# Kernel optimization log

Hardware: AMD Instinct MI355X
Metric: run time of the kernel (lower is better)

The kernel has to match this reference:

```python
import jax, jax.numpy as jnp
import numpy as np

N_REF = 4

def setup_inputs() -> dict:
    key = jax.random.key(0)
    ks = jax.random.split(key, 6)
    B, C, H, W = 4, 256, 64, 64
    s = 1.0 / np.sqrt(C)
    return {
        'x': jax.random.normal(ks[0], (B, C, H, W), jnp.float32),
        'Wq': jax.random.normal(ks[1], (C, C), jnp.float32) * s,
        'bq': jnp.zeros((C,), jnp.float32),
        'Wk': jax.random.normal(ks[2], (C, C), jnp.float32) * s,
        'bk': jnp.zeros((C,), jnp.float32),
        'Wv': jax.random.normal(ks[3], (C, C), jnp.float32) * s,
        'bv': jnp.zeros((C,), jnp.float32),
        'Woff': jax.random.normal(ks[4], (2 * N_REF, C), jnp.float32) * s,
        'boff': jnp.zeros((2 * N_REF,), jnp.float32),
    }

def _proj(x, W, b):
    # 1x1 conv == channel-mixing linear: [B,C,H,W] -> [B,O,H,W]
    return jnp.einsum('oc,bchw->bohw', W, x) + b[None, :, None, None]

def reference(x, Wq, bq, Wk, bk, Wv, bv, Woff, boff):
    B, C, H, W = x.shape
    n = N_REF
    HW = H * W
    Q = _proj(x, Wq, bq)
    K = _proj(x, Wk, bk)
    V = _proj(x, Wv, bv)
    offsets = _proj(Q, Woff, boff).reshape(B, n, 2, H, W)
    grid_h, grid_w = jnp.meshgrid(jnp.arange(H), jnp.arange(W), indexing='ij')
    ref_x = jnp.clip(jnp.round(grid_w[None, None] + offsets[:, :, 0]).astype(jnp.int32), 0, W - 1)
    ref_y = jnp.clip(jnp.round(grid_h[None, None] + offsets[:, :, 1]).astype(jnp.int32), 0, H - 1)
    ref_idx = (ref_y * W + ref_x).reshape(B, n, HW)          # [B,n,HW]
    K_flat = K.reshape(B, C, HW)
    V_flat = V.reshape(B, C, HW)
    # gather along spatial dim -> [B,C,n,HW]
    idx = ref_idx[:, None, :, :]                              # [B,1,n,HW]
    K_g = jnp.take_along_axis(K_flat[:, :, None, :], idx, axis=3)
    V_g = jnp.take_along_axis(V_flat[:, :, None, :], idx, axis=3)
    Q_flat = Q.reshape(B, C, HW)
    attn = jnp.einsum('bch,bcnh->bnh', Q_flat, K_g)
    attn = jax.nn.softmax(attn, axis=1)
    out = jnp.einsum('bnh,bcnh->bch', attn, V_g)
    return out.reshape(B, C, H, W)
```

## Files before the change

kernel.cpp:

```cpp
#include <hip/hip_runtime.h>
#include <math.h>

#define B_DIM   4
#define C_DIM   256
#define H_DIM   64
#define W_DIM   64
#define HW_DIM  4096
#define NPIX    (B_DIM * HW_DIM)
#define NREF    4
#define NJ      10

typedef unsigned short u16;
typedef __attribute__((ext_vector_type(4))) unsigned short u16x4;
typedef __attribute__((ext_vector_type(8))) unsigned short u16x8;
typedef __attribute__((ext_vector_type(8))) short bf16x8;
typedef __attribute__((ext_vector_type(4))) float f32x4;

__device__ __forceinline__ u16 bf16_rne(float f) {
    unsigned u = __float_as_uint(f);
    u = u + 0x7FFFu + ((u >> 16) & 1u);
    return (u16)(u >> 16);
}
__device__ __forceinline__ float bf16_tof(u16 h) {
    return __uint_as_float(((unsigned)h) << 16);
}
__device__ __forceinline__ void gload16(const void* g, void* l) {
    __builtin_amdgcn_global_load_lds(
        (const __attribute__((address_space(1))) void*)g,
        (__attribute__((address_space(3))) void*)l, 16, 0, 0);
}

__global__ __launch_bounds__(256) void prep_kernel(
    const float* __restrict__ Wq, const float* __restrict__ bq,
    const float* __restrict__ Wk, const float* __restrict__ bk,
    const float* __restrict__ Wv,
    const float* __restrict__ Woff, const float* __restrict__ boff,
    double* __restrict__ Weffp, double* __restrict__ beff,
    u16* __restrict__ Bswh, u16* __restrict__ Bswl)
{
    const int bx = blockIdx.x;
    const int t  = threadIdx.x;

    if (bx < 4 * NJ) {
        const int j  = bx >> 2;
        const int q  = bx & 3;
        const int o0 = q * 64;
        const float* Avec = (j < 8) ? (Woff + j * C_DIM) : ((j == 8) ? bq : bk);
        const float* Bmat = (j == 8) ? Wk : Wq;
        double s0 = 0, s1 = 0, s2 = 0, s3 = 0;
        for (int o = o0; o < o0 + 64; o += 4) {
            s0 += (double)Avec[o + 0] * (double)Bmat[(size_t)(o + 0) * C_DIM + t];
            s1 += (double)Avec[o + 1] * (double)Bmat[(size_t)(o + 1) * C_DIM + t];
            s2 += (double)Avec[o + 2] * (double)Bmat[(size_t)(o + 2) * C_DIM + t];
            s3 += (double)Avec[o + 3] * (double)Bmat[(size_t)(o + 3) * C_DIM + t];
        }
        Weffp[(size_t)(q * NJ + j) * C_DIM + t] = (s0 + s1) + (s2 + s3);

        if (q == 0 && j <= 8) {
            __shared__ double red[256];
            red[t] = (j < 8) ? (double)Woff[j * C_DIM + t] * (double)bq[t]
                             : (double)bq[t] * (double)bk[t];
            __syncthreads();
            for (int st = 128; st > 0; st >>= 1) {
                if (t < st) red[t] += red[t + st];
                __syncthreads();
            }
            if (t == 0) beff[j] = (j < 8) ? red[0] + (double)boff[j] : red[0];
        }
    } else if (bx < 72) {
        __shared__ float wq_s[64][32];
        __shared__ float wk_s[64][64];
        const int sub   = bx - 40;
        const int T     = sub >> 2;
        const int nsub  = sub & 3;
        const int ntile = T >> 2;
        const int kt    = T & 3;
        const int nb    = ntile * 128 + nsub * 32;
        const int kb    = kt * 64;

        const int tx = t & 15;
        const int ty = t >> 4;

        float acc[2][4] = {};

        for (int oc = 0; oc < 4; ++oc) {
            const int o0 = oc * 64;
#pragma unroll
            for (int i = 0; i < 2; ++i) {
                const int s = i * 256 + t;
                const int row = s >> 3, c4 = (s & 7) * 4;
                *(float4*)&wq_s[row][c4] =
                    *(const float4*)(Wq + (size_t)(o0 + row) * C_DIM + nb + c4);
            }
#pragma unroll
            for (int i = 0; i < 4; ++i) {
                const int s = i * 256 + t;
                const int row = s >> 4, c4 = (s & 15) * 4;
                *(float4*)&wk_s[row][c4] =
                    *(const float4*)(Wk + (size_t)(o0 + row) * C_DIM + kb + c4);
            }
            __syncthreads();
#pragma unroll 4
            for (int oo = 0; oo < 64; ++oo) {
                const float2 a = *(const float2*)&wq_s[oo][ty * 2];
                const float4 b4 = *(const float4*)&wk_s[oo][tx * 4];
                acc[0][0] = fmaf(a.x, b4.x, acc[0][0]);
                acc[0][1] = fmaf(a.x, b4.y, acc[0][1]);
                acc[0][2] = fmaf(a.x, b4.z, acc[0][2]);
                acc[0][3] = fmaf(a.x, b4.w, acc[0][3]);
                acc[1][0] = fmaf(a.y, b4.x, acc[1][0]);
                acc[1][1] = fmaf(a.y, b4.y, acc[1][1]);
                acc[1][2] = fmaf(a.y, b4.z, acc[1][2]);
                acc[1][3] = fmaf(a.y, b4.w, acc[1][3]);
            }
            __syncthreads();
        }

        u16* dh = Bswh + (size_t)T * 8192;
        u16* dl = Bswl + (size_t)T * 8192;
#pragma unroll
        for (int j = 0; j < 2; ++j) {
            const int rimg = nsub * 32 + ty * 2 + j;
            const int base = rimg * 64 + (((tx >> 1) ^ (rimg & 7)) * 8) + (tx & 1) * 4;
            u16x4 hv, lv;
#pragma unroll
            for (int i = 0; i < 4; ++i) {
                hv[i] = bf16_rne(acc[j][i]);
                lv[i] = bf16_rne(acc[j][i] - bf16_tof(hv[i]));
            }
            *(u16x4*)(dh + base) = hv;
            *(u16x4*)(dl + base) = lv;
        }
    } else {
        const int ti    = bx - 72;
        const int kt    = ti & 3;
        const int ntile = (ti >> 2) & 1;
        const int Timg  = 8 + ti;
        const int n0 = ntile * 128, k0 = kt * 64;
        u16* dh = Bswh + (size_t)Timg * 8192;
#pragma unroll
        for (int it = 0; it < 4; ++it) {
            const int s   = it * 256 + t;
            const int row = s >> 3;
            const int ch  = s & 7;
            const int kk  = k0 + (ch ^ (row & 7)) * 8;
            const float4 w0 = *(const float4*)(Wv + (size_t)(n0 + row) * C_DIM + kk);
            const float4 w1 = *(const float4*)(Wv + (size_t)(n0 + row) * C_DIM + kk + 4);
            u16x8 hv;
            hv[0] = bf16_rne(w0.x); hv[1] = bf16_rne(w0.y);
            hv[2] = bf16_rne(w0.z); hv[3] = bf16_rne(w0.w);
            hv[4] = bf16_rne(w1.x); hv[5] = bf16_rne(w1.y);
            hv[6] = bf16_rne(w1.z); hv[7] = bf16_rne(w1.w);
            *(u16x8*)(dh + (size_t)s * 8) = hv;
        }
    }
}

__global__ __launch_bounds__(256) void xsplit_kernel(
    const float* __restrict__ x, const double* __restrict__ Weffp,
    u16* __restrict__ xh, u16* __restrict__ xl, double* __restrict__ part)
{
    __shared__ float  tile[64][65];
    __shared__ double wf[NJ][64];
    const int b   = blockIdx.z;
    const int cy  = blockIdx.y;
    const int c0  = cy * 64;
    const int hw0 = blockIdx.x * 64;
    const int t   = threadIdx.x;
    const int r4  = t >> 6;
    const int col = t & 63;

#pragma unroll
    for (int i = 0; i < 16; ++i) {
        const int row = i * 4 + r4;
        tile[row][col] = x[((size_t)b * C_DIM + c0 + row) * HW_DIM + hw0 + col];
    }
    for (int d = t; d < NJ * 64; d += 256) {
        const int jj = d >> 6, cc = d & 63;
        ((double*)wf)[d] = Weffp[(size_t)(0 * NJ + jj) * C_DIM + c0 + cc]
                         + Weffp[(size_t)(1 * NJ + jj) * C_DIM + c0 + cc]
                         + Weffp[(size_t)(2 * NJ + jj) * C_DIM + c0 + cc]
                         + Weffp[(size_t)(3 * NJ + jj) * C_DIM + c0 + cc];
    }
    __syncthreads();

#pragma unroll
    for (int i = 0; i < 16; ++i) {
        const int hwr = i * 4 + r4;
        const float v = tile[col][hwr];
        const u16 h = bf16_rne(v);
        const float lo = v - bf16_tof(h);
        const size_t o = ((size_t)b * HW_DIM + hw0 + hwr) * C_DIM + c0 + col;
        xh[o] = h;
        xl[o] = bf16_rne(lo);
    }

    const int p = col, g = r4;
    double a0 = 0, a1 = 0, a2 = 0;
    for (int c = 0; c < 64; ++c) {
        const double xv = (double)tile[c][p];
        a0 += wf[2 * g][c] * xv;
        a1 += wf[2 * g + 1][c] * xv;
        if (g < 2) a2 += wf[8 + g][c] * xv;
    }
    const int pix = b * HW_DIM + hw0 + p;
    part[(size_t)(cy * NJ + 2 * g) * NPIX + pix]     = a0;
    part[(size_t)(cy * NJ + 2 * g + 1) * NPIX + pix] = a1;
    if (g < 2) part[(size_t)(cy * NJ + 8 + g) * NPIX + pix] = a2;
}

__global__ __launch_bounds__(256) void idx_kernel(
    const double* __restrict__ part, const double* __restrict__ beff,
    int* __restrict__ idx_buf, float* __restrict__ kqf, float* __restrict__ vqf)
{
    const int pix = blockIdx.x * 256 + threadIdx.x;
    const int hw  = pix & (HW_DIM - 1);
    const int h   = hw >> 6;
    const int w   = hw & 63;

    double o[8];
#pragma unroll
    for (int j = 0; j < 8; ++j)
        o[j] = part[(size_t)(0 * NJ + j) * NPIX + pix] + part[(size_t)(1 * NJ + j) * NPIX + pix]
             + part[(size_t)(2 * NJ + j) * NPIX + pix] + part[(size_t)(3 * NJ + j) * NPIX + pix]
             + beff[j];

    int r[NREF];
#pragma unroll
    for (int n = 0; n < NREF; ++n) {
        const float ox = (float)o[2 * n];
        const float oy = (float)o[2 * n + 1];
        int rx = (int)rintf((float)w + ox);
        int ry = (int)rintf((float)h + oy);
        rx = min(max(rx, 0), W_DIM - 1);
        ry = min(max(ry, 0), H_DIM - 1);
        r[n] = ry * W_DIM + rx;
    }
    int4 outv; outv.x = r[0]; outv.y = r[1]; outv.z = r[2]; outv.w = r[3];
    *(int4*)(idx_buf + (size_t)pix * 4) = outv;

    const double kq = part[(size_t)(0 * NJ + 8) * NPIX + pix] + part[(size_t)(1 * NJ + 8) * NPIX + pix]
                    + part[(size_t)(2 * NJ + 8) * NPIX + pix] + part[(size_t)(3 * NJ + 8) * NPIX + pix];
    const double vq = part[(size_t)(0 * NJ + 9) * NPIX + pix] + part[(size_t)(1 * NJ + 9) * NPIX + pix]
                    + part[(size_t)(2 * NJ + 9) * NPIX + pix] + part[(size_t)(3 * NJ + 9) * NPIX + pix]
                    + beff[8];
    kqf[pix] = (float)kq;
    vqf[pix] = (float)vq;
}

__global__ __launch_bounds__(256) void qkv_mfma(
    const u16* __restrict__ xh, const u16* __restrict__ xl,
    const u16* __restrict__ Bswh, const u16* __restrict__ Bswl,
    const float* __restrict__ bv,
    float* __restrict__ Kpt, u16* __restrict__ Vtb)
{
    const int mat = blockIdx.x & 1;
    const int m0  = (blockIdx.x >> 1) * 64;
    const bool three = (mat == 0);

    __shared__ u16 lds[40960];
    u16* Ah = lds;
    u16* Al = lds + 4096;
    u16* Bh = lds + 8192;
    u16* Bl = lds + 24576;

    const int t    = threadIdx.x;
    const int lane = t & 63;
    const int wv   = t >> 6;
    const int wm   = (wv >> 1) * 32;
    const int wn   = (wv & 1) * 128;

    f32x4 acc[2][8] = {};

    for (int kt = 0; kt < 4; ++kt) {
        const int k0 = kt * 64;

#pragma unroll
        for (int it = 0; it < 2; ++it) {
            const int s   = it * 256 + t;
            const int row = s >> 3;
            const int sch = (s & 7) ^ (row & 7);
            const size_t goff = (size_t)(m0 + row) * C_DIM + k0 + sch * 8;
            gload16(xh + goff, (char*)Ah + s * 16);
            if (three) gload16(xl + goff, (char*)Al + s * 16);
        }
#pragma unroll
        for (int it = 0; it < 8; ++it) {
            const int s  = it * 256 + t;
            const int ni = s >> 10;
            const int sl = s & 1023;
            const size_t Tb = (size_t)((mat * 2 + ni) * 4 + kt) * 8192;
            gload16(Bswh + Tb + (size_t)sl * 8, (char*)Bh + s * 16);
            if (three) gload16(Bswl + Tb + (size_t)sl * 8, (char*)Bl + s * 16);
        }
        __syncthreads();

#pragma unroll
        for (int ks = 0; ks < 2; ++ks) {
            bf16x8 afh[2], afl[2];
#pragma unroll
            for (int mt = 0; mt < 2; ++mt) {
                const int row = wm + mt * 16 + (lane & 15);
                const int ch  = (ks * 4 + (lane >> 4)) ^ (row & 7);
                const int off = row * 128 + ch * 16;
                afh[mt] = *(const bf16x8*)((const char*)Ah + off);
                if (three) afl[mt] = *(const bf16x8*)((const char*)Al + off);
            }
#pragma unroll
            for (int ng = 0; ng < 2; ++ng) {
                bf16x8 bfh[4], bfl[4];
#pragma unroll
                for (int nt = 0; nt < 4; ++nt) {
                    const int row = wn + ng * 64 + nt * 16 + (lane & 15);
                    const int ch  = (ks * 4 + (lane >> 4)) ^ (row & 7);
                    const int off = row * 128 + ch * 16;
                    bfh[nt] = *(const bf16x8*)((const char*)Bh + off);
                    if (three) bfl[nt] = *(const bf16x8*)((const char*)Bl + off);
                }
#pragma unroll
                for (int mt = 0; mt < 2; ++mt)
#pragma unroll
                    for (int nt = 0; nt < 4; ++nt) {
                        f32x4 a = acc[mt][ng * 4 + nt];
                        a = __builtin_amdgcn_mfma_f32_16x16x32_bf16(afh[mt], bfh[nt], a, 0, 0, 0);
                        if (three) {
                            a = __builtin_amdgcn_mfma_f32_16x16x32_bf16(afh[mt], bfl[nt], a, 0, 0, 0);
                            a = __builtin_amdgcn_mfma_f32_16x16x32_bf16(afl[mt], bfh[nt], a, 0, 0, 0);
                        }
                        acc[mt][ng * 4 + nt] = a;
                    }
            }
        }
        __syncthreads();
    }

    const int col = lane & 15;
    const int rg  = (lane >> 4) * 4;
#pragma unroll
    for (int ng = 0; ng < 2; ++ng)
#pragma unroll
        for (int nt = 0; nt < 4; ++nt) {
            const int n = wn + ng * 64 + nt * 16 + col;
            const float bias = mat ? bv[n] : 0.0f;
#pragma unroll
            for (int mt = 0; mt < 2; ++mt) {
                const int m = m0 + wm + mt * 16 + rg;
#pragma unroll
                for (int r = 0; r < 4; ++r) {
                    const float v = acc[mt][ng * 4 + nt][r] + bias;
                    if (mat) Vtb[(size_t)(m + r) * C_DIM + n] = bf16_rne(v);
                    else     Kpt[(size_t)(m + r) * C_DIM + n] = v;
                }
            }
        }
}

__global__ __launch_bounds__(1024) void attn_kernel(
    const u16*   __restrict__ xh,
    const u16*   __restrict__ xl,
    const float* __restrict__ Kpt,
    const u16*   __restrict__ Vtb,
    const int*   __restrict__ idx_buf,
    const float* __restrict__ kqf,
    const float* __restrict__ vqf,
    float* __restrict__ out)
{
    __shared__ float trans[16][260];

    const int t    = threadIdx.x;
    const int wave = t >> 6;
    const int lane = t & 63;

    const int pix0 = blockIdx.x * 16;
    const int b    = pix0 / HW_DIM;
    const int hw   = (pix0 % HW_DIM) + wave;
    const int pix  = b * HW_DIM + hw;

    const u16x4 hv = *(const u16x4*)(xh + (size_t)pix * C_DIM + lane * 4);
    const u16x4 lv = *(const u16x4*)(xl + (size_t)pix * C_DIM + lane * 4);
    float q[4];
#pragma unroll
    for (int i = 0; i < 4; ++i) q[i] = bf16_tof(hv[i]) + bf16_tof(lv[i]);

    const int4 iv = *(const int4*)(idx_buf + (size_t)pix * 4);
    int idx[NREF] = {iv.x, iv.y, iv.z, iv.w};
    const float vq = vqf[pix];

    float logit[NREF];
#pragma unroll
    for (int n = 0; n < NREF; ++n) {
        const float* krow = Kpt + ((size_t)b * HW_DIM + idx[n]) * C_DIM;
        float4 kv = *(const float4*)(krow + lane * 4);
        float lp = fmaf(q[3], kv.w, fmaf(q[2], kv.z, fmaf(q[1], kv.y, q[0] * kv.x)));
#pragma unroll
        for (int off = 1; off < 64; off <<= 1) lp += __shfl_xor(lp, off);
        logit[n] = lp + kqf[(size_t)b * HW_DIM + idx[n]] + vq;
    }

    float mx = fmaxf(fmaxf(logit[0], logit[1]), fmaxf(logit[2], logit[3]));
    float e[NREF], s = 0.0f;
#pragma unroll
    for (int n = 0; n < NREF; ++n) { e[n] = expf(logit[n] - mx); s += e[n]; }
    float wgt[NREF];
#pragma unroll
    for (int n = 0; n < NREF; ++n) wgt[n] = e[n] / s;

    float o4[4] = {0.f, 0.f, 0.f, 0.f};
#pragma unroll
    for (int n = 0; n < NREF; ++n) {
        const u16x4 vv = *(const u16x4*)(Vtb + ((size_t)b * HW_DIM + idx[n]) * C_DIM + lane * 4);
        o4[0] = fmaf(wgt[n], bf16_tof(vv[0]), o4[0]);
        o4[1] = fmaf(wgt[n], bf16_tof(vv[1]), o4[1]);
        o4[2] = fmaf(wgt[n], bf16_tof(vv[2]), o4[2]);
        o4[3] = fmaf(wgt[n], bf16_tof(vv[3]), o4[3]);
    }

    *(float4*)&trans[wave][lane * 4] = *(float4*)o4;
    __syncthreads();

    float* ob = out + (size_t)b * C_DIM * HW_DIM + (pix0 % HW_DIM);
    const int px = t & 15;
#pragma unroll
    for (int cc = 0; cc < C_DIM; cc += 64) {
        const int c = cc + (t >> 4);
        ob[(size_t)c * HW_DIM + px] = trans[px][c];
    }
}

extern "C" void kernel_launch(void* const* d_in, const int* in_sizes, int n_in,
                              void* d_out, int out_size, void* d_ws, size_t ws_size,
                              hipStream_t stream) {
    const float* x    = (const float*)d_in[0];
    const float* Wq   = (const float*)d_in[1];
    const float* bq   = (const float*)d_in[2];
    const float* Wk   = (const float*)d_in[3];
    const float* bk   = (const float*)d_in[4];
    const float* Wv   = (const float*)d_in[5];
    const float* bv   = (const float*)d_in[6];
    const float* Woff = (const float*)d_in[7];
    const float* boff = (const float*)d_in[8];
    float* out = (float*)d_out;

    char* ws = (char*)d_ws;
    float*  Kpt   = (float*)ws;
    u16*    Vtb   = (u16*)  (ws + (size_t)16 * 1024 * 1024);
    u16*    xh    = (u16*)  (ws + (size_t)48 * 1024 * 1024);
    u16*    xl    = (u16*)  (ws + (size_t)56 * 1024 * 1024);
    char*   aux   = ws + (size_t)64 * 1024 * 1024;
    double* Weffp = (double*)(aux);
    double* beff  = (double*)(aux + 128 * 1024);
    int*    idxb  = (int*)   (aux + 192 * 1024);
    float*  kqf   = (float*) (aux + 448 * 1024);
    float*  vqf   = (float*) (aux + 512 * 1024);
    u16*    Bswh  = (u16*)   (aux + 576 * 1024);
    u16*    Bswl  = (u16*)   (aux + 832 * 1024);
    double* part  = (double*)(aux + 2 * 1024 * 1024);

    prep_kernel<<<dim3(80), dim3(256), 0, stream>>>(
        Wq, bq, Wk, bk, Wv, Woff, boff, Weffp, beff, Bswh, Bswl);
    xsplit_kernel<<<dim3(HW_DIM / 64, C_DIM / 64, B_DIM), dim3(256), 0, stream>>>(
        x, Weffp, xh, xl, part);
    idx_kernel<<<dim3(NPIX / 256), dim3(256), 0, stream>>>(part, beff, idxb, kqf, vqf);
    qkv_mfma<<<dim3((NPIX / 64) * 2), dim3(256), 0, stream>>>(
        xh, xl, Bswh, Bswl, bv, Kpt, Vtb);
    attn_kernel<<<dim3(NPIX / 16), dim3(1024), 0, stream>>>(
        xh, xl, Kpt, Vtb, idxb, kqf, vqf, out);
}
```

Before: 64.67 us.

## Fuse xsplit with index computation and compute K and V in one GEMM block

The xsplit and idx kernels are merged. Each block now loops over all four channel chunks for 32 pixels and reduces the offset partial sums in shared memory, so the double-precision partial buffer round trip through global memory and one launch go away. The QKV GEMM kernel now computes both the K (three-pass split bf16) and V (single-pass) outputs for a 32-row tile inside the same block, reusing the loaded A tile. The cost is fewer pixels per block in the fused kernel, serial channel chunks with extra barriers, and a smaller M tile that lowers B-operand reuse in the GEMM.

New measurement: 105.0 us. 62.3% more time.

```diff
diff --git a/kernel.cpp b/kernel.cpp
--- a/kernel.cpp
+++ b/kernel.cpp
@@ -156,96 +156,93 @@
     }
 }
 
-__global__ __launch_bounds__(256) void xsplit_kernel(
+__global__ __launch_bounds__(256) void xsplit_idx_kernel(
     const float* __restrict__ x, const double* __restrict__ Weffp,
-    u16* __restrict__ xh, u16* __restrict__ xl, double* __restrict__ part)
-{
-    __shared__ float  tile[64][65];
-    __shared__ double wf[NJ][64];
-    const int b   = blockIdx.z;
-    const int cy  = blockIdx.y;
-    const int c0  = cy * 64;
-    const int hw0 = blockIdx.x * 64;
-    const int t   = threadIdx.x;
-    const int r4  = t >> 6;
-    const int col = t & 63;
-
-#pragma unroll
-    for (int i = 0; i < 16; ++i) {
-        const int row = i * 4 + r4;
-        tile[row][col] = x[((size_t)b * C_DIM + c0 + row) * HW_DIM + hw0 + col];
-    }
-    for (int d = t; d < NJ * 64; d += 256) {
-        const int jj = d >> 6, cc = d & 63;
-        ((double*)wf)[d] = Weffp[(size_t)(0 * NJ + jj) * C_DIM + c0 + cc]
-                         + Weffp[(size_t)(1 * NJ + jj) * C_DIM + c0 + cc]
-                         + Weffp[(size_t)(2 * NJ + jj) * C_DIM + c0 + cc]
-                         + Weffp[(size_t)(3 * NJ + jj) * C_DIM + c0 + cc];
-    }
-    __syncthreads();
-
-#pragma unroll
-    for (int i = 0; i < 16; ++i) {
-        const int hwr = i * 4 + r4;
-        const float v = tile[col][hwr];
-        const u16 h = bf16_rne(v);
-        const float lo = v - bf16_tof(h);
-        const size_t o = ((size_t)b * HW_DIM + hw0 + hwr) * C_DIM + c0 + col;
-        xh[o] = h;
-        xl[o] = bf16_rne(lo);
-    }
-
-    const int p = col, g = r4;
-    double a0 = 0, a1 = 0, a2 = 0;
-    for (int c = 0; c < 64; ++c) {
-        const double xv = (double)tile[c][p];
-        a0 += wf[2 * g][c] * xv;
-        a1 += wf[2 * g + 1][c] * xv;
-        if (g < 2) a2 += wf[8 + g][c] * xv;
-    }
-    const int pix = b * HW_DIM + hw0 + p;
-    part[(size_t)(cy * NJ + 2 * g) * NPIX + pix]     = a0;
-    part[(size_t)(cy * NJ + 2 * g + 1) * NPIX + pix] = a1;
-    if (g < 2) part[(size_t)(cy * NJ + 8 + g) * NPIX + pix] = a2;
-}
-
-__global__ __launch_bounds__(256) void idx_kernel(
-    const double* __restrict__ part, const double* __restrict__ beff,
+    const double* __restrict__ beff,
+    u16* __restrict__ xh, u16* __restrict__ xl,
     int* __restrict__ idx_buf, float* __restrict__ kqf, float* __restrict__ vqf)
 {
-    const int pix = blockIdx.x * 256 + threadIdx.x;
-    const int hw  = pix & (HW_DIM - 1);
-    const int h   = hw >> 6;
-    const int w   = hw & 63;
-
-    double o[8];
-#pragma unroll
-    for (int j = 0; j < 8; ++j)
-        o[j] = part[(size_t)(0 * NJ + j) * NPIX + pix] + part[(size_t)(1 * NJ + j) * NPIX + pix]
-             + part[(size_t)(2 * NJ + j) * NPIX + pix] + part[(size_t)(3 * NJ + j) * NPIX + pix]
-             + beff[j];
-
-    int r[NREF];
-#pragma unroll
-    for (int n = 0; n < NREF; ++n) {
-        const float ox = (float)o[2 * n];
-        const float oy = (float)o[2 * n + 1];
-        int rx = (int)rintf((float)w + ox);
-        int ry = (int)rintf((float)h + oy);
-        rx = min(max(rx, 0), W_DIM - 1);
-        ry = min(max(ry, 0), H_DIM - 1);
-        r[n] = ry * W_DIM + rx;
-    }
-    int4 outv; outv.x = r[0]; outv.y = r[1]; outv.z = r[2]; outv.w = r[3];
-    *(int4*)(idx_buf + (size_t)pix * 4) = outv;
-
-    const double kq = part[(size_t)(0 * NJ + 8) * NPIX + pix] + part[(size_t)(1 * NJ + 8) * NPIX + pix]
-                    + part[(size_t)(2 * NJ + 8) * NPIX + pix] + part[(size_t)(3 * NJ + 8) * NPIX + pix];
-    const double vq = part[(size_t)(0 * NJ + 9) * NPIX + pix] + part[(size_t)(1 * NJ + 9) * NPIX + pix]
-                    + part[(size_t)(2 * NJ + 9) * NPIX + pix] + part[(size_t)(3 * NJ + 9) * NPIX + pix]
-                    + beff[8];
-    kqf[pix] = (float)kq;
-    vqf[pix] = (float)vq;
+    __shared__ float  tile[64][33];
+    __shared__ double wf[NJ][64];
+    __shared__ double osum[NJ][32];
+
+    const int b   = blockIdx.y;
+    const int hw0 = blockIdx.x * 32;
+    const int t   = threadIdx.x;
+
+    const int p  = t & 31;
+    const int g  = t >> 5;
+    const int cl = t & 63;
+    const int gg = t >> 6;
+
+    double pj[4], pj2[4];
+
+    for (int cy = 0; cy < 4; ++cy) {
+        const int c0 = cy * 64;
+        if (cy) __syncthreads();
+
+#pragma unroll
+        for (int i = 0; i < 8; ++i) {
+            const int s = i * 256 + t;
+            const int row = s >> 5;
+            const int pp  = s & 31;
+            tile[row][pp] = x[((size_t)b * C_DIM + c0 + row) * HW_DIM + hw0 + pp];
+        }
+        for (int d = t; d < NJ * 64; d += 256) {
+            const int jj = d >> 6, cc = d & 63;
+            ((double*)wf)[d] = Weffp[(size_t)(0 * NJ + jj) * C_DIM + c0 + cc]
+                             + Weffp[(size_t)(1 * NJ + jj) * C_DIM + c0 + cc]
+                             + Weffp[(size_t)(2 * NJ + jj) * C_DIM + c0 + cc]
+                             + Weffp[(size_t)(3 * NJ + jj) * C_DIM + c0 + cc];
+        }
+        __syncthreads();
+
+#pragma unroll
+        for (int i = 0; i < 8; ++i) {
+            const int hwr = i * 4 + gg;
+            const float v = tile[cl][hwr];
+            const u16 hbits = bf16_rne(v);
+            const float lo = v - bf16_tof(hbits);
+            const size_t o = ((size_t)b * HW_DIM + hw0 + hwr) * C_DIM + c0 + cl;
+            xh[o] = hbits;
+            xl[o] = bf16_rne(lo);
+        }
+
+        double a0 = 0, a1 = 0;
+        for (int c = 0; c < 64; ++c) {
+            const double xv = (double)tile[c][p];
+            a0 += wf[g][c] * xv;
+            if (g < 2) a1 += wf[8 + g][c] * xv;
+        }
+        pj[cy]  = a0;
+        pj2[cy] = a1;
+    }
+
+    osum[g][p] = ((pj[0] + pj[1]) + pj[2]) + pj[3];
+    if (g < 2) osum[8 + g][p] = ((pj2[0] + pj2[1]) + pj2[2]) + pj2[3];
+    __syncthreads();
+
+    if (t < 32) {
+        const int hw  = hw0 + t;
+        const int pix = b * HW_DIM + hw;
+        const int h   = hw >> 6;
+        const int w   = hw & 63;
+        int r[NREF];
+#pragma unroll
+        for (int n = 0; n < NREF; ++n) {
+            const float ox = (float)(osum[2 * n][t]     + beff[2 * n]);
+            const float oy = (float)(osum[2 * n + 1][t] + beff[2 * n + 1]);
+            int rx = (int)rintf((float)w + ox);
+            int ry = (int)rintf((float)h + oy);
+            rx = min(max(rx, 0), W_DIM - 1);
+            ry = min(max(ry, 0), H_DIM - 1);
+            r[n] = ry * W_DIM + rx;
+        }
+        int4 outv; outv.x = r[0]; outv.y = r[1]; outv.z = r[2]; outv.w = r[3];
+        *(int4*)(idx_buf + (size_t)pix * 4) = outv;
+        kqf[pix] = (float)osum[8][t];
+        vqf[pix] = (float)(osum[9][t] + beff[8]);
+    }
 }
 
 __global__ __launch_bounds__(256) void qkv_mfma(
@@ -254,82 +251,103 @@
     const float* __restrict__ bv,
     float* __restrict__ Kpt, u16* __restrict__ Vtb)
 {
-    const int mat = blockIdx.x & 1;
-    const int m0  = (blockIdx.x >> 1) * 64;
-    const bool three = (mat == 0);
-
-    __shared__ u16 lds[40960];
+    const int m0 = blockIdx.x * 32;
+
+    __shared__ u16 lds[36864];
     u16* Ah = lds;
-    u16* Al = lds + 4096;
-    u16* Bh = lds + 8192;
-    u16* Bl = lds + 24576;
+    u16* Al = lds + 2048;
+    u16* Bh = lds + 4096;
+    u16* Bl = lds + 20480;
 
     const int t    = threadIdx.x;
     const int lane = t & 63;
     const int wv   = t >> 6;
-    const int wm   = (wv >> 1) * 32;
+    const int wm   = (wv >> 1) * 16;
     const int wn   = (wv & 1) * 128;
 
-    f32x4 acc[2][8] = {};
+    f32x4 accK[8] = {};
+    f32x4 accV[8] = {};
 
     for (int kt = 0; kt < 4; ++kt) {
         const int k0 = kt * 64;
 
-#pragma unroll
-        for (int it = 0; it < 2; ++it) {
-            const int s   = it * 256 + t;
+        {
+            const int s   = t;
             const int row = s >> 3;
             const int sch = (s & 7) ^ (row & 7);
             const size_t goff = (size_t)(m0 + row) * C_DIM + k0 + sch * 8;
             gload16(xh + goff, (char*)Ah + s * 16);
-            if (three) gload16(xl + goff, (char*)Al + s * 16);
+            gload16(xl + goff, (char*)Al + s * 16);
         }
 #pragma unroll
         for (int it = 0; it < 8; ++it) {
             const int s  = it * 256 + t;
             const int ni = s >> 10;
             const int sl = s & 1023;
-            const size_t Tb = (size_t)((mat * 2 + ni) * 4 + kt) * 8192;
+            const size_t Tb = (size_t)(ni * 4 + kt) * 8192;
             gload16(Bswh + Tb + (size_t)sl * 8, (char*)Bh + s * 16);
-            if (three) gload16(Bswl + Tb + (size_t)sl * 8, (char*)Bl + s * 16);
+            gload16(Bswl + Tb + (size_t)sl * 8, (char*)Bl + s * 16);
         }
         __syncthreads();
 
 #pragma unroll
         for (int ks = 0; ks < 2; ++ks) {
-            bf16x8 afh[2], afl[2];
-#pragma unroll
-            for (int mt = 0; mt < 2; ++mt) {
-                const int row = wm + mt * 16 + (lane & 15);
+            bf16x8 afh, afl;
+            {
+                const int row = wm + (lane & 15);
                 const int ch  = (ks * 4 + (lane >> 4)) ^ (row & 7);
                 const int off = row * 128 + ch * 16;
-                afh[mt] = *(const bf16x8*)((const char*)Ah + off);
-                if (three) afl[mt] = *(const bf16x8*)((const char*)Al + off);
-            }
-#pragma unroll
-            for (int ng = 0; ng < 2; ++ng) {
-                bf16x8 bfh[4], bfl[4];
+                afh = *(const bf16x8*)((const char*)Ah + off);
+                afl = *(const bf16x8*)((const char*)Al + off);
+            }
+#pragma unroll
+            for (int ng = 0; ng < 2; ++ng)
 #pragma unroll
                 for (int nt = 0; nt < 4; ++nt) {
                     const int row = wn + ng * 64 + nt * 16 + (lane & 15);
                     const int ch  = (ks * 4 + (lane >> 4)) ^ (row & 7);
                     const int off = row * 128 + ch * 16;
-                    bfh[nt] = *(const bf16x8*)((const char*)Bh + off);
-                    if (three) bfl[nt] = *(const bf16x8*)((const char*)Bl + off);
+                    const bf16x8 bh = *(const bf16x8*)((const char*)Bh + off);
+                    const bf16x8 bl = *(const bf16x8*)((const char*)Bl + off);
+                    f32x4 a = accK[ng * 4 + nt];
+                    a = __builtin_amdgcn_mfma_f32_16x16x32_bf16(afh, bh, a, 0, 0, 0);
+                    a = __builtin_amdgcn_mfma_f32_16x16x32_bf16(afh, bl, a, 0, 0, 0);
+                    a = __builtin_amdgcn_mfma_f32_16x16x32_bf16(afl, bh, a, 0, 0, 0);
+                    accK[ng * 4 + nt] = a;
                 }
-#pragma unroll
-                for (int mt = 0; mt < 2; ++mt)
-#pragma unroll
-                    for (int nt = 0; nt < 4; ++nt) {
-                        f32x4 a = acc[mt][ng * 4 + nt];
-                        a = __builtin_amdgcn_mfma_f32_16x16x32_bf16(afh[mt], bfh[nt], a, 0, 0, 0);
-                        if (three) {
-                            a = __builtin_amdgcn_mfma_f32_16x16x32_bf16(afh[mt], bfl[nt], a, 0, 0, 0);
-                            a = __builtin_amdgcn_mfma_f32_16x16x32_bf16(afl[mt], bfh[nt], a, 0, 0, 0);
-                        }
-                        acc[mt][ng * 4 + nt] = a;
-                    }
-            }
+        }
+        __syncthreads();
+
+#pragma unroll
+        for (int it = 0; it < 8; ++it) {
+            const int s  = it * 256 + t;
+            const int ni = s >> 10;
+            const int sl = s & 1023;
+            const size_t Tb = (size_t)(8 + ni * 4 + kt) * 8192;
+            gload16(Bswh + Tb + (size_t)sl * 8, (char*)Bh + s * 16);
+        }
+        __syncthreads();
+
+#pragma unroll
+        for (int ks = 0; ks < 2; ++ks) {
+            bf16x8 afh;
+            {
+                const int row = wm + (lane & 15);
+                const int ch  = (ks * 4 + (lane >> 4)) ^ (row & 7);
+                const int off = row * 128 + ch * 16;
+                afh = *(const bf16x8*)((const char*)Ah + off);
+            }
+#pragma unroll
+            for (int ng = 0; ng < 2; ++ng)
+#pragma unroll
+                for (int nt = 0; nt < 4; ++nt) {
+                    const int row = wn + ng * 64 + nt * 16 + (lane & 15);
+                    const int ch  = (ks * 4 + (lane >> 4)) ^ (row & 7);
+                    const int off = row * 128 + ch * 16;
+                    const bf16x8 bh = *(const bf16x8*)((const char*)Bh + off);
+                    accV[ng * 4 + nt] =
+                        __builtin_amdgcn_mfma_f32_16x16x32_bf16(afh, bh, accV[ng * 4 + nt], 0, 0, 0);
+                }
         }
         __syncthreads();
     }
@@ -341,16 +359,12 @@
 #pragma unroll
         for (int nt = 0; nt < 4; ++nt) {
             const int n = wn + ng * 64 + nt * 16 + col;
-            const float bias = mat ? bv[n] : 0.0f;
-#pragma unroll
-            for (int mt = 0; mt < 2; ++mt) {
-                const int m = m0 + wm + mt * 16 + rg;
-#pragma unroll
-                for (int r = 0; r < 4; ++r) {
-                    const float v = acc[mt][ng * 4 + nt][r] + bias;
-                    if (mat) Vtb[(size_t)(m + r) * C_DIM + n] = bf16_rne(v);
-                    else     Kpt[(size_t)(m + r) * C_DIM + n] = v;
-                }
+            const float bias = bv[n];
+            const int m = m0 + wm + rg;
+#pragma unroll
+            for (int r = 0; r < 4; ++r) {
+                Kpt[(size_t)(m + r) * C_DIM + n] = accK[ng * 4 + nt][r];
+                Vtb[(size_t)(m + r) * C_DIM + n] = bf16_rne(accV[ng * 4 + nt][r] + bias);
             }
         }
 }
@@ -454,14 +468,12 @@
     float*  vqf   = (float*) (aux + 512 * 1024);
     u16*    Bswh  = (u16*)   (aux + 576 * 1024);
     u16*    Bswl  = (u16*)   (aux + 832 * 1024);
-    double* part  = (double*)(aux + 2 * 1024 * 1024);
 
     prep_kernel<<<dim3(80), dim3(256), 0, stream>>>(
         Wq, bq, Wk, bk, Wv, Woff, boff, Weffp, beff, Bswh, Bswl);
-    xsplit_kernel<<<dim3(HW_DIM / 64, C_DIM / 64, B_DIM), dim3(256), 0, stream>>>(
-        x, Weffp, xh, xl, part);
-    idx_kernel<<<dim3(NPIX / 256), dim3(256), 0, stream>>>(part, beff, idxb, kqf, vqf);
-    qkv_mfma<<<dim3((NPIX / 64) * 2), dim3(256), 0, stream>>>(
+    xsplit_idx_kernel<<<dim3(HW_DIM / 32, B_DIM), dim3(256), 0, stream>>>(
+        x, Weffp, beff, xh, xl, idxb, kqf, vqf);
+    qkv_mfma<<<dim3(NPIX / 32), dim3(256), 0, stream>>>(
         xh, xl, Bswh, Bswl, bv, Kpt, Vtb);
     attn_kernel<<<dim3(NPIX / 16), dim3(1024), 0, stream>>>(
         xh, xl, Kpt, Vtb, idxb, kqf, vqf, out);
```

## Fuse K and V projections into one block sharing the loaded x tile

Applied to the files above, without the earlier changes.

The QKV GEMM kernel no longer splits K and V across separate blocks. Each block now takes 32 rows and computes both the 3-pass split-bf16 K product and the 1-pass V product from a single staged x tile, reloading only the B weight tile for V. This removes the imbalance between the heavy K blocks and light V blocks and avoids loading x twice. In exchange, the M tile per block is halved, giving less weight reuse, and there are extra syncs and weight loads per k-step.

Result: no change. 64.99 us (+0.5%).

```diff
diff --git a/kernel.cpp b/kernel.cpp
--- a/kernel.cpp
+++ b/kernel.cpp
@@ -254,82 +254,103 @@
     const float* __restrict__ bv,
     float* __restrict__ Kpt, u16* __restrict__ Vtb)
 {
-    const int mat = blockIdx.x & 1;
-    const int m0  = (blockIdx.x >> 1) * 64;
-    const bool three = (mat == 0);
-
-    __shared__ u16 lds[40960];
+    const int m0 = blockIdx.x * 32;
+
+    __shared__ u16 lds[36864];
     u16* Ah = lds;
-    u16* Al = lds + 4096;
-    u16* Bh = lds + 8192;
-    u16* Bl = lds + 24576;
+    u16* Al = lds + 2048;
+    u16* Bh = lds + 4096;
+    u16* Bl = lds + 20480;
 
     const int t    = threadIdx.x;
     const int lane = t & 63;
     const int wv   = t >> 6;
-    const int wm   = (wv >> 1) * 32;
+    const int wm   = (wv >> 1) * 16;
     const int wn   = (wv & 1) * 128;
 
-    f32x4 acc[2][8] = {};
+    f32x4 accK[8] = {};
+    f32x4 accV[8] = {};
 
     for (int kt = 0; kt < 4; ++kt) {
         const int k0 = kt * 64;
 
-#pragma unroll
-        for (int it = 0; it < 2; ++it) {
-            const int s   = it * 256 + t;
+        {
+            const int s   = t;
             const int row = s >> 3;
             const int sch = (s & 7) ^ (row & 7);
             const size_t goff = (size_t)(m0 + row) * C_DIM + k0 + sch * 8;
             gload16(xh + goff, (char*)Ah + s * 16);
-            if (three) gload16(xl + goff, (char*)Al + s * 16);
+            gload16(xl + goff, (char*)Al + s * 16);
         }
 #pragma unroll
         for (int it = 0; it < 8; ++it) {
             const int s  = it * 256 + t;
             const int ni = s >> 10;
             const int sl = s & 1023;
-            const size_t Tb = (size_t)((mat * 2 + ni) * 4 + kt) * 8192;
+            const size_t Tb = (size_t)(ni * 4 + kt) * 8192;
             gload16(Bswh + Tb + (size_t)sl * 8, (char*)Bh + s * 16);
-            if (three) gload16(Bswl + Tb + (size_t)sl * 8, (char*)Bl + s * 16);
+            gload16(Bswl + Tb + (size_t)sl * 8, (char*)Bl + s * 16);
         }
         __syncthreads();
 
 #pragma unroll
         for (int ks = 0; ks < 2; ++ks) {
-            bf16x8 afh[2], afl[2];
-#pragma unroll
-            for (int mt = 0; mt < 2; ++mt) {
-                const int row = wm + mt * 16 + (lane & 15);
+            bf16x8 afh, afl;
+            {
+                const int row = wm + (lane & 15);
                 const int ch  = (ks * 4 + (lane >> 4)) ^ (row & 7);
                 const int off = row * 128 + ch * 16;
-                afh[mt] = *(const bf16x8*)((const char*)Ah + off);
-                if (three) afl[mt] = *(const bf16x8*)((const char*)Al + off);
-            }
-#pragma unroll
-            for (int ng = 0; ng < 2; ++ng) {
-                bf16x8 bfh[4], bfl[4];
+                afh = *(const bf16x8*)((const char*)Ah + off);
+                afl = *(const bf16x8*)((const char*)Al + off);
+            }
+#pragma unroll
+            for (int ng = 0; ng < 2; ++ng)
 #pragma unroll
                 for (int nt = 0; nt < 4; ++nt) {
                     const int row = wn + ng * 64 + nt * 16 + (lane & 15);
                     const int ch  = (ks * 4 + (lane >> 4)) ^ (row & 7);
                     const int off = row * 128 + ch * 16;
-                    bfh[nt] = *(const bf16x8*)((const char*)Bh + off);
-                    if (three) bfl[nt] = *(const bf16x8*)((const char*)Bl + off);
+                    const bf16x8 bh = *(const bf16x8*)((const char*)Bh + off);
+                    const bf16x8 bl = *(const bf16x8*)((const char*)Bl + off);
+                    f32x4 a = accK[ng * 4 + nt];
+                    a = __builtin_amdgcn_mfma_f32_16x16x32_bf16(afh, bh, a, 0, 0, 0);
+                    a = __builtin_amdgcn_mfma_f32_16x16x32_bf16(afh, bl, a, 0, 0, 0);
+                    a = __builtin_amdgcn_mfma_f32_16x16x32_bf16(afl, bh, a, 0, 0, 0);
+                    accK[ng * 4 + nt] = a;
                 }
-#pragma unroll
-                for (int mt = 0; mt < 2; ++mt)
-#pragma unroll
-                    for (int nt = 0; nt < 4; ++nt) {
-                        f32x4 a = acc[mt][ng * 4 + nt];
-                        a = __builtin_amdgcn_mfma_f32_16x16x32_bf16(afh[mt], bfh[nt], a, 0, 0, 0);
-                        if (three) {
-                            a = __builtin_amdgcn_mfma_f32_16x16x32_bf16(afh[mt], bfl[nt], a, 0, 0, 0);
-                            a = __builtin_amdgcn_mfma_f32_16x16x32_bf16(afl[mt], bfh[nt], a, 0, 0, 0);
-                        }
-                        acc[mt][ng * 4 + nt] = a;
-                    }
-            }
+        }
+        __syncthreads();
+
+#pragma unroll
+        for (int it = 0; it < 8; ++it) {
+            const int s  = it * 256 + t;
+            const int ni = s >> 10;
+            const int sl = s & 1023;
+            const size_t Tb = (size_t)(8 + ni * 4 + kt) * 8192;
+            gload16(Bswh + Tb + (size_t)sl * 8, (char*)Bh + s * 16);
+        }
+        __syncthreads();
+
+#pragma unroll
+        for (int ks = 0; ks < 2; ++ks) {
+            bf16x8 afh;
+            {
+                const int row = wm + (lane & 15);
+                const int ch  = (ks * 4 + (lane >> 4)) ^ (row & 7);
+                const int off = row * 128 + ch * 16;
+                afh = *(const bf16x8*)((const char*)Ah + off);
+            }
+#pragma unroll
+            for (int ng = 0; ng < 2; ++ng)
+#pragma unroll
+                for (int nt = 0; nt < 4; ++nt) {
+                    const int row = wn + ng * 64 + nt * 16 + (lane & 15);
+                    const int ch  = (ks * 4 + (lane >> 4)) ^ (row & 7);
+                    const int off = row * 128 + ch * 16;
+                    const bf16x8 bh = *(const bf16x8*)((const char*)Bh + off);
+                    accV[ng * 4 + nt] =
+                        __builtin_amdgcn_mfma_f32_16x16x32_bf16(afh, bh, accV[ng * 4 + nt], 0, 0, 0);
+                }
         }
         __syncthreads();
     }
@@ -341,16 +362,12 @@
 #pragma unroll
         for (int nt = 0; nt < 4; ++nt) {
             const int n = wn + ng * 64 + nt * 16 + col;
-            const float bias = mat ? bv[n] : 0.0f;
-#pragma unroll
-            for (int mt = 0; mt < 2; ++mt) {
-                const int m = m0 + wm + mt * 16 + rg;
-#pragma unroll
-                for (int r = 0; r < 4; ++r) {
-                    const float v = acc[mt][ng * 4 + nt][r] + bias;
-                    if (mat) Vtb[(size_t)(m + r) * C_DIM + n] = bf16_rne(v);
-                    else     Kpt[(size_t)(m + r) * C_DIM + n] = v;
-                }
+            const float bias = bv[n];
+            const int m = m0 + wm + rg;
+#pragma unroll
+            for (int r = 0; r < 4; ++r) {
+                Kpt[(size_t)(m + r) * C_DIM + n] = accK[ng * 4 + nt][r];
+                Vtb[(size_t)(m + r) * C_DIM + n] = bf16_rne(accV[ng * 4 + nt][r] + bias);
             }
         }
 }
@@ -461,7 +478,7 @@
     xsplit_kernel<<<dim3(HW_DIM / 64, C_DIM / 64, B_DIM), dim3(256), 0, stream>>>(
         x, Weffp, xh, xl, part);
     idx_kernel<<<dim3(NPIX / 256), dim3(256), 0, stream>>>(part, beff, idxb, kqf, vqf);
-    qkv_mfma<<<dim3((NPIX / 64) * 2), dim3(256), 0, stream>>>(
+    qkv_mfma<<<dim3(NPIX / 32), dim3(256), 0, stream>>>(
         xh, xl, Bswh, Bswl, bv, Kpt, Vtb);
     attn_kernel<<<dim3(NPIX / 16), dim3(1024), 0, stream>>>(
         xh, xl, Kpt, Vtb, idxb, kqf, vqf, out);
```
